# Kernel optimization log

Hardware: AMD Instinct MI355X
Metric: run time of the kernel (lower is better)

## Reference

```python
import jax, jax.numpy as jnp
import numpy as np

B = 16
PATCH_NUM = 32      # L of inter branch
PATCH_SIZE = 128    # L of intra branch
WIN_SIZE = PATCH_NUM * PATCH_SIZE  # 4096
H = 8
E = 64


def setup_inputs() -> dict:
    key = jax.random.key(0)
    ks = jax.random.split(key, 6)
    return {
        "q_inter": jax.random.normal(ks[0], (B, PATCH_NUM, H, E), jnp.float32),
        "k_inter": jax.random.normal(ks[1], (B, PATCH_NUM, H, E), jnp.float32),
        "v_inter": jax.random.normal(ks[2], (B, PATCH_NUM, H, E), jnp.float32),
        "q_intra": jax.random.normal(ks[3], (B, PATCH_SIZE, H, E), jnp.float32),
        "k_intra": jax.random.normal(ks[4], (B, PATCH_SIZE, H, E), jnp.float32),
        "v_intra": jax.random.normal(ks[5], (B, PATCH_SIZE, H, E), jnp.float32),
    }


def _full_attention(q, k, v):
    # q,k,v: [B, L, H, E]; full softmax attention, scale = 1/sqrt(E)
    scale = 1.0 / jnp.sqrt(jnp.asarray(q.shape[-1], q.dtype))
    score = jnp.einsum('blhe,bshe->bhls', q, k) * scale
    att = jax.nn.softmax(score, axis=-1)  # dropout is identity in eval mode
    return jnp.einsum('bhls,bshd->blhd', att, v)


def reference(q_inter, k_inter, v_inter, q_intra, k_intra, v_intra):
    V_inter = _full_attention(q_inter, k_inter, v_inter)  # [B, patch_num, H, E]
    V_intra = _full_attention(q_intra, k_intra, v_intra)  # [B, patch_size, H, E]
    # einops repeat 'b pn h d -> b (pn ps) h d': each patch repeated ps times
    V_inter_up = jnp.repeat(V_inter, PATCH_SIZE, axis=1)  # [B, win_size, H, E]
    # einops repeat 'b ps h d -> b (ps pn) h d': each position repeated pn times
    V_intra_up = jnp.repeat(V_intra, PATCH_NUM, axis=1)   # [B, win_size, H, E]
    return V_inter_up + V_intra_up
```

## Files before the change

kernel.cpp:

```cpp
#include <hip/hip_runtime.h>


#define NH 8
#define NE 64
#define ROWSTRIDE (NH * NE)

typedef float vf4 __attribute__((ext_vector_type(4)));

__device__ __forceinline__ float dot4(const float4 a, const float4 b) {
    return a.x * b.x + a.y * b.y + a.z * b.z + a.w * b.w;
}

__device__ __forceinline__ float readlane_f(float v, int lane) {
    return __uint_as_float(__builtin_amdgcn_readlane(__float_as_uint(v), lane));
}

__global__ __launch_bounds__(256, 2) void attn_combined(
    const float* __restrict__ qI, const float* __restrict__ kI, const float* __restrict__ vI,
    const float* __restrict__ qT, const float* __restrict__ kT, const float* __restrict__ vT,
    float* __restrict__ wsSum)
{
    __shared__ __align__(16) float sKs[128 * 68];
    __shared__ __align__(16) float sVs[128 * 64];
    __shared__ __align__(16) float sQs[32 * 68];
    __shared__ __align__(16) float sIO[8 * 68];

    const int tid  = threadIdx.x;
    const int bid  = blockIdx.x;
    const int tile = bid & 3;
    const int h    = (bid >> 2) & 7;
    const int b    = bid >> 5;
    const int r0   = tile * 32;
    const int pn0  = tile * 8;

    {
        const float* kg = kI + ((size_t)b * 32 * NH + h) * NE;
        const float* vg = vI + ((size_t)b * 32 * NH + h) * NE;
        float* dK = sKs;
        float* dV = sKs + 32 * 68;
        for (int idx = tid; idx < 32 * 16; idx += 256) {
            const int row = idx >> 4;
            const int f   = (idx & 15) * 4;
            *(float4*)&dK[row * 68 + f] = *(const float4*)(kg + (size_t)row * ROWSTRIDE + f);
            *(float4*)&dV[row * 64 + f] = *(const float4*)(vg + (size_t)row * ROWSTRIDE + f);
        }
        const float* vgT = vT + ((size_t)b * 128 * NH + h) * NE;
        for (int idx = tid; idx < 128 * 16; idx += 256) {
            const int row = idx >> 4;
            const int f   = (idx & 15) * 4;
            *(float4*)&sVs[row * 64 + f] = *(const float4*)(vgT + (size_t)row * ROWSTRIDE + f);
        }
        const float* qgT = qT + ((size_t)(b * 128 + r0) * NH + h) * NE;
        for (int idx = tid; idx < 32 * 16; idx += 256) {
            const int row = idx >> 4;
            const int f   = (idx & 15) * 4;
            *(float4*)&sQs[row * 68 + f] = *(const float4*)(qgT + (size_t)row * ROWSTRIDE + f);
        }
    }
    __syncthreads();

    {
        const int rg = tid >> 5;
        const int ln = tid & 31;
        const float* dK = sKs;
        const float* dV = sKs + 32 * 68;

        const float* qrow = qI + ((size_t)(b * 32 + pn0 + rg) * NH + h) * NE;
        float s = 0.f;
        #pragma unroll
        for (int e = 0; e < NE; e += 4) {
            const float4 qv = *(const float4*)(qrow + e);
            const float4 kv = *(const float4*)&dK[ln * 68 + e];
            s += dot4(qv, kv);
        }
        s *= 0.125f;
        float m = s;
        #pragma unroll
        for (int msk = 1; msk < 32; msk <<= 1) m = fmaxf(m, __shfl_xor(m, msk));
        const float pe = __expf(s - m);
        float sum = pe;
        #pragma unroll
        for (int msk = 1; msk < 32; msk <<= 1) sum += __shfl_xor(sum, msk);
        const float pn = pe / sum;

        const int hw = tid & 32;
        float o0 = 0.f, o1 = 0.f;
        #pragma unroll 8
        for (int c = 0; c < 32; c++) {
            const float pc = __shfl(pn, hw + c);
            const float2 v = *(const float2*)&dV[c * 64 + ln * 2];
            o0 += pc * v.x;
            o1 += pc * v.y;
        }
        sIO[rg * 68 + ln * 2]     = o0;
        sIO[rg * 68 + ln * 2 + 1] = o1;
    }
    __syncthreads();

    {
        const float* kgT = kT + ((size_t)b * 128 * NH + h) * NE;
        for (int idx = tid; idx < 128 * 16; idx += 256) {
            const int row = idx >> 4;
            const int f   = (idx & 15) * 4;
            *(float4*)&sKs[row * 68 + f] = *(const float4*)(kgT + (size_t)row * ROWSTRIDE + f);
        }
    }
    __syncthreads();

    const int rg = tid >> 5;
    const int cg = tid & 31;
    const int rr = rg * 4;
    float acc[4][4];
    #pragma unroll
    for (int i = 0; i < 4; i++)
        #pragma unroll
        for (int j = 0; j < 4; j++) acc[i][j] = 0.f;

    #pragma unroll
    for (int e = 0; e < NE; e += 4) {
        float4 qv[4], kv[4];
        #pragma unroll
        for (int i = 0; i < 4; i++) qv[i] = *(const float4*)&sQs[(rr + i) * 68 + e];
        #pragma unroll
        for (int j = 0; j < 4; j++) kv[j] = *(const float4*)&sKs[(cg + j * 32) * 68 + e];
        #pragma unroll
        for (int i = 0; i < 4; i++)
            #pragma unroll
            for (int j = 0; j < 4; j++)
                acc[i][j] += dot4(qv[i], kv[j]);
    }

    float p[4][4];
    #pragma unroll
    for (int i = 0; i < 4; i++) {
        float m = acc[i][0] * 0.125f;
        #pragma unroll
        for (int j = 1; j < 4; j++) m = fmaxf(m, acc[i][j] * 0.125f);
        #pragma unroll
        for (int msk = 1; msk < 32; msk <<= 1) m = fmaxf(m, __shfl_xor(m, msk));
        float s = 0.f;
        #pragma unroll
        for (int j = 0; j < 4; j++) { p[i][j] = __expf(acc[i][j] * 0.125f - m); s += p[i][j]; }
        #pragma unroll
        for (int msk = 1; msk < 32; msk <<= 1) s += __shfl_xor(s, msk);
        const float inv = 1.f / s;
        #pragma unroll
        for (int j = 0; j < 4; j++) p[i][j] *= inv;
    }

    const int lane = tid & 63;
    const int w    = tid >> 6;
    float accE[8] = {0.f, 0.f, 0.f, 0.f, 0.f, 0.f, 0.f, 0.f};

    for (int j = 0; j < 4; j++) {
        #pragma unroll
        for (int cc = 0; cc < 32; cc++) {
            const float v = sVs[(j * 32 + cc) * 64 + lane];
            #pragma unroll
            for (int i = 0; i < 8; i++) {
                const float pc = readlane_f(p[i & 3][j], (i >> 2) * 32 + cc);
                accE[i] = fmaf(pc, v, accE[i]);
            }
        }
    }

    #pragma unroll
    for (int i = 0; i < 8; i++) {
        const float vin = sIO[(2 * w + (i >> 2)) * 68 + lane];
        const int   row = r0 + 8 * w + i;
        wsSum[((size_t)(b * 128 + row) * NH + h) * NE + lane] = accE[i] + vin;
    }
}

__global__ __launch_bounds__(256) void duplicate_kernel(
    const float4* __restrict__ ws, float* __restrict__ out)
{
    const int t  = blockIdx.x * 256 + threadIdx.x;
    const int e4 = t & 15;
    const int h  = (t >> 4) & 7;
    const int pi = (t >> 7) & 127;
    const int b  = t >> 14;

    const float4 a = ws[((b * 128 + pi) * NH + h) * 16 + e4];
    vf4 s; s.x = a.x; s.y = a.y; s.z = a.z; s.w = a.w;

    float* o = out + ((((size_t)b * 4096 + pi * 32) * NH + h) * 16 + e4) * 4;
    #pragma unroll
    for (int j = 0; j < 32; j++)
        __builtin_nontemporal_store(s, (vf4*)(o + (size_t)j * ROWSTRIDE));
}

extern "C" void kernel_launch(void* const* d_in, const int* in_sizes, int n_in,
                              void* d_out, int out_size, void* d_ws, size_t ws_size,
                              hipStream_t stream) {
    const float* q_inter = (const float*)d_in[0];
    const float* k_inter = (const float*)d_in[1];
    const float* v_inter = (const float*)d_in[2];
    const float* q_intra = (const float*)d_in[3];
    const float* k_intra = (const float*)d_in[4];
    const float* v_intra = (const float*)d_in[5];
    float* out = (float*)d_out;
    float* ws  = (float*)d_ws;

    attn_combined<<<512, 256, 0, stream>>>(
        q_inter, k_inter, v_inter, q_intra, k_intra, v_intra, ws);

    duplicate_kernel<<<1024, 256, 0, stream>>>((const float4*)ws, out);
}
```

Baseline: 178.0 us.

## Compute intra-branch attention with bf16 MFMA and shared-memory softmax

Replaces the scalar fp32 QK^T and PV loops of the intra attention with bf16 MFMA 16x16x32 instructions. K, Q, P and a transposed V are converted to bf16 in shared memory, and the shared-memory layout is repacked into one overlapping byte buffer. Softmax now runs on scores staged in LDS, with 8 lanes per row. This cuts ALU work, but it lowers precision to bf16 and adds extra barriers and conversions. The output is dominated by the separate duplicate kernel that writes a 128 MB output, so the attention part is a small share of the total.

```diff
diff --git a/kernel.cpp b/kernel.cpp
--- a/kernel.cpp
+++ b/kernel.cpp
@@ -3,27 +3,34 @@
 
 #define NH 8
 #define NE 64
-#define ROWSTRIDE (NH * NE)
-
-typedef float vf4 __attribute__((ext_vector_type(4)));
+#define ROWSTRIDE 512
+
+typedef float  vf4 __attribute__((ext_vector_type(4)));
+typedef short  v8s __attribute__((ext_vector_type(8)));
 
 __device__ __forceinline__ float dot4(const float4 a, const float4 b) {
     return a.x * b.x + a.y * b.y + a.z * b.z + a.w * b.w;
 }
 
-__device__ __forceinline__ float readlane_f(float v, int lane) {
-    return __uint_as_float(__builtin_amdgcn_readlane(__float_as_uint(v), lane));
-}
-
-__global__ __launch_bounds__(256, 2) void attn_combined(
+__device__ __forceinline__ unsigned short f2bf(float f) {
+    unsigned int u = __float_as_uint(f);
+    u += 0x7fff + ((u >> 16) & 1);
+    return (unsigned short)(u >> 16);
+}
+
+#define SMEM_BYTES 51328
+#define OFF_QB  18432
+#define OFF_R2  23040
+#define OFF_IV  31744
+#define OFF_P   40448
+#define OFF_IO  49152
+
+__global__ __launch_bounds__(256, 2) void attn_mfma(
     const float* __restrict__ qI, const float* __restrict__ kI, const float* __restrict__ vI,
     const float* __restrict__ qT, const float* __restrict__ kT, const float* __restrict__ vT,
     float* __restrict__ wsSum)
 {
-    __shared__ __align__(16) float sKs[128 * 68];
-    __shared__ __align__(16) float sVs[128 * 64];
-    __shared__ __align__(16) float sQs[32 * 68];
-    __shared__ __align__(16) float sIO[8 * 68];
+    __shared__ __align__(16) char smem[SMEM_BYTES];
 
     const int tid  = threadIdx.x;
     const int bid  = blockIdx.x;
@@ -36,34 +43,44 @@
     {
         const float* kg = kI + ((size_t)b * 32 * NH + h) * NE;
         const float* vg = vI + ((size_t)b * 32 * NH + h) * NE;
-        float* dK = sKs;
-        float* dV = sKs + 32 * 68;
+        float* dK = (float*)(smem + OFF_R2);
+        float* dV = (float*)(smem + OFF_IV);
         for (int idx = tid; idx < 32 * 16; idx += 256) {
             const int row = idx >> 4;
             const int f   = (idx & 15) * 4;
             *(float4*)&dK[row * 68 + f] = *(const float4*)(kg + (size_t)row * ROWSTRIDE + f);
             *(float4*)&dV[row * 64 + f] = *(const float4*)(vg + (size_t)row * ROWSTRIDE + f);
         }
-        const float* vgT = vT + ((size_t)b * 128 * NH + h) * NE;
+    }
+    __syncthreads();
+
+    {
+        const float* kgT = kT + ((size_t)b * 128 * NH + h) * NE;
+        unsigned short* wKb = (unsigned short*)smem;
         for (int idx = tid; idx < 128 * 16; idx += 256) {
             const int row = idx >> 4;
             const int f   = (idx & 15) * 4;
-            *(float4*)&sVs[row * 64 + f] = *(const float4*)(vgT + (size_t)row * ROWSTRIDE + f);
+            const float4 v = *(const float4*)(kgT + (size_t)row * ROWSTRIDE + f);
+            ushort4 pk; pk.x = f2bf(v.x); pk.y = f2bf(v.y); pk.z = f2bf(v.z); pk.w = f2bf(v.w);
+            *(ushort4*)(wKb + row * 72 + f) = pk;
         }
         const float* qgT = qT + ((size_t)(b * 128 + r0) * NH + h) * NE;
+        unsigned short* wQb = (unsigned short*)(smem + OFF_QB);
         for (int idx = tid; idx < 32 * 16; idx += 256) {
             const int row = idx >> 4;
             const int f   = (idx & 15) * 4;
-            *(float4*)&sQs[row * 68 + f] = *(const float4*)(qgT + (size_t)row * ROWSTRIDE + f);
-        }
-    }
-    __syncthreads();
+            const float4 v = *(const float4*)(qgT + (size_t)row * ROWSTRIDE + f);
+            ushort4 pk; pk.x = f2bf(v.x); pk.y = f2bf(v.y); pk.z = f2bf(v.z); pk.w = f2bf(v.w);
+            *(ushort4*)(wQb + row * 72 + f) = pk;
+        }
+    }
 
     {
         const int rg = tid >> 5;
         const int ln = tid & 31;
-        const float* dK = sKs;
-        const float* dV = sKs + 32 * 68;
+        const float* dK  = (const float*)(smem + OFF_R2);
+        const float* dV  = (const float*)(smem + OFF_IV);
+        float*       sIO = (float*)(smem + OFF_IO);
 
         const float* qrow = qI + ((size_t)(b * 32 + pn0 + rg) * NH + h) * NE;
         float s = 0.f;
@@ -98,77 +115,120 @@
     __syncthreads();
 
     {
-        const float* kgT = kT + ((size_t)b * 128 * NH + h) * NE;
+        const float* vgT = vT + ((size_t)b * 128 * NH + h) * NE;
+        unsigned short* wVb = (unsigned short*)(smem + OFF_R2);
         for (int idx = tid; idx < 128 * 16; idx += 256) {
-            const int row = idx >> 4;
-            const int f   = (idx & 15) * 4;
-            *(float4*)&sKs[row * 68 + f] = *(const float4*)(kgT + (size_t)row * ROWSTRIDE + f);
-        }
-    }
-    __syncthreads();
-
-    const int rg = tid >> 5;
-    const int cg = tid & 31;
-    const int rr = rg * 4;
-    float acc[4][4];
+            const int c = idx >> 4;
+            const int f = (idx & 15) * 4;
+            const float4 v = *(const float4*)(vgT + (size_t)c * ROWSTRIDE + f);
+            const float arr[4] = { v.x, v.y, v.z, v.w };
+            #pragma unroll
+            for (int i = 0; i < 4; i++) {
+                const int j = (c + i) & 3;
+                wVb[(f + j) * 136 + c] = f2bf(arr[j]);
+            }
+        }
+    }
+    __syncthreads();
+
+    const int lane = tid & 63;
+    const int ln15 = lane & 15;
+    const int quad = lane >> 4;
+    const int w    = tid >> 6;
+    const int mt   = w & 1;
+    const int ntb  = (w >> 1) * 4;
+
+    vf4 accS[4];
     #pragma unroll
-    for (int i = 0; i < 4; i++)
-        #pragma unroll
-        for (int j = 0; j < 4; j++) acc[i][j] = 0.f;
-
-    #pragma unroll
-    for (int e = 0; e < NE; e += 4) {
-        float4 qv[4], kv[4];
-        #pragma unroll
-        for (int i = 0; i < 4; i++) qv[i] = *(const float4*)&sQs[(rr + i) * 68 + e];
-        #pragma unroll
-        for (int j = 0; j < 4; j++) kv[j] = *(const float4*)&sKs[(cg + j * 32) * 68 + e];
-        #pragma unroll
-        for (int i = 0; i < 4; i++)
-            #pragma unroll
-            for (int j = 0; j < 4; j++)
-                acc[i][j] += dot4(qv[i], kv[j]);
-    }
-
-    float p[4][4];
-    #pragma unroll
-    for (int i = 0; i < 4; i++) {
-        float m = acc[i][0] * 0.125f;
-        #pragma unroll
-        for (int j = 1; j < 4; j++) m = fmaxf(m, acc[i][j] * 0.125f);
-        #pragma unroll
-        for (int msk = 1; msk < 32; msk <<= 1) m = fmaxf(m, __shfl_xor(m, msk));
+    for (int t = 0; t < 4; t++) accS[t] = (vf4){0.f, 0.f, 0.f, 0.f};
+    {
+        const unsigned short* sKb = (const unsigned short*)smem;
+        const unsigned short* sQb = (const unsigned short*)(smem + OFF_QB);
+        #pragma unroll
+        for (int kt = 0; kt < 2; kt++) {
+            const v8s aQ = *(const v8s*)(sQb + (mt * 16 + ln15) * 72 + kt * 32 + quad * 8);
+            #pragma unroll
+            for (int t = 0; t < 4; t++) {
+                const v8s bK = *(const v8s*)(sKb + ((ntb + t) * 16 + ln15) * 72 + kt * 32 + quad * 8);
+                accS[t] = __builtin_amdgcn_mfma_f32_16x16x32_bf16(aQ, bK, accS[t], 0, 0, 0);
+            }
+        }
+    }
+    __syncthreads();
+
+    {
+        float* sS = (float*)smem;
+        #pragma unroll
+        for (int t = 0; t < 4; t++)
+            #pragma unroll
+            for (int reg = 0; reg < 4; reg++)
+                sS[(mt * 16 + quad * 4 + reg) * 132 + (ntb + t) * 16 + ln15]
+                    = accS[t][reg] * 0.125f;
+    }
+    __syncthreads();
+
+    {
+        const float* sS = (const float*)smem;
+        unsigned short* sP = (unsigned short*)(smem + OFF_P);
+        const int r   = tid >> 3;
+        const int sub = tid & 7;
+        float vals[16];
+        const float* Srow = sS + r * 132 + sub * 16;
+        #pragma unroll
+        for (int c4 = 0; c4 < 4; c4++) {
+            const float4 v = *(const float4*)(Srow + c4 * 4);
+            vals[c4*4+0] = v.x; vals[c4*4+1] = v.y; vals[c4*4+2] = v.z; vals[c4*4+3] = v.w;
+        }
+        float m = vals[0];
+        #pragma unroll
+        for (int i = 1; i < 16; i++) m = fmaxf(m, vals[i]);
+        #pragma unroll
+        for (int msk = 1; msk < 8; msk <<= 1) m = fmaxf(m, __shfl_xor(m, msk));
         float s = 0.f;
         #pragma unroll
-        for (int j = 0; j < 4; j++) { p[i][j] = __expf(acc[i][j] * 0.125f - m); s += p[i][j]; }
-        #pragma unroll
-        for (int msk = 1; msk < 32; msk <<= 1) s += __shfl_xor(s, msk);
+        for (int i = 0; i < 16; i++) { vals[i] = __expf(vals[i] - m); s += vals[i]; }
+        #pragma unroll
+        for (int msk = 1; msk < 8; msk <<= 1) s += __shfl_xor(s, msk);
         const float inv = 1.f / s;
         #pragma unroll
-        for (int j = 0; j < 4; j++) p[i][j] *= inv;
-    }
-
-    const int lane = tid & 63;
-    const int w    = tid >> 6;
-    float accE[8] = {0.f, 0.f, 0.f, 0.f, 0.f, 0.f, 0.f, 0.f};
-
-    for (int j = 0; j < 4; j++) {
-        #pragma unroll
-        for (int cc = 0; cc < 32; cc++) {
-            const float v = sVs[(j * 32 + cc) * 64 + lane];
-            #pragma unroll
-            for (int i = 0; i < 8; i++) {
-                const float pc = readlane_f(p[i & 3][j], (i >> 2) * 32 + cc);
-                accE[i] = fmaf(pc, v, accE[i]);
-            }
-        }
-    }
-
-    #pragma unroll
-    for (int i = 0; i < 8; i++) {
-        const float vin = sIO[(2 * w + (i >> 2)) * 68 + lane];
-        const int   row = r0 + 8 * w + i;
-        wsSum[((size_t)(b * 128 + row) * NH + h) * NE + lane] = accE[i] + vin;
+        for (int c4 = 0; c4 < 4; c4++) {
+            ushort4 pk;
+            pk.x = f2bf(vals[c4*4+0] * inv); pk.y = f2bf(vals[c4*4+1] * inv);
+            pk.z = f2bf(vals[c4*4+2] * inv); pk.w = f2bf(vals[c4*4+3] * inv);
+            *(ushort4*)(sP + r * 136 + sub * 16 + c4 * 4) = pk;
+        }
+    }
+    __syncthreads();
+
+    {
+        const unsigned short* sVb = (const unsigned short*)(smem + OFF_R2);
+        const unsigned short* sP  = (const unsigned short*)(smem + OFF_P);
+        const float*          sIO = (const float*)(smem + OFF_IO);
+        const int neb = (w >> 1) * 2;
+
+        vf4 accO[2];
+        accO[0] = (vf4){0.f, 0.f, 0.f, 0.f};
+        accO[1] = (vf4){0.f, 0.f, 0.f, 0.f};
+        #pragma unroll
+        for (int kt = 0; kt < 4; kt++) {
+            const v8s aP = *(const v8s*)(sP + (mt * 16 + ln15) * 136 + kt * 32 + quad * 8);
+            #pragma unroll
+            for (int t = 0; t < 2; t++) {
+                const v8s bV = *(const v8s*)(sVb + ((neb + t) * 16 + ln15) * 136 + kt * 32 + quad * 8);
+                accO[t] = __builtin_amdgcn_mfma_f32_16x16x32_bf16(aP, bV, accO[t], 0, 0, 0);
+            }
+        }
+
+        #pragma unroll
+        for (int t = 0; t < 2; t++) {
+            const int e   = (neb + t) * 16 + ln15;
+            const float vin = sIO[(mt * 4 + quad) * 68 + e];
+            #pragma unroll
+            for (int reg = 0; reg < 4; reg++) {
+                const int row = r0 + mt * 16 + quad * 4 + reg;
+                wsSum[((size_t)(b * 128 + row) * NH + h) * NE + e] = accO[t][reg] + vin;
+            }
+        }
     }
 }
 
@@ -202,7 +262,7 @@
     float* out = (float*)d_out;
     float* ws  = (float*)d_ws;
 
-    attn_combined<<<512, 256, 0, stream>>>(
+    attn_mfma<<<512, 256, 0, stream>>>(
         q_inter, k_inter, v_inter, q_intra, k_intra, v_intra, ws);
 
     duplicate_kernel<<<1024, 256, 0, stream>>>((const float4*)ws, out);
```

New measurement: 170.9 us. -4.0%, faster.
